# Performance work log

Measured on AMD Instinct MI355X. Metric: run time of the kernel, lower is better.

The kernel has to match this reference:

```python
import jax, jax.numpy as jnp
import numpy as np

HEADS = 8
DIM_HEAD = 64
SCALE = DIM_HEAD ** -0.5


def setup_inputs() -> dict:
    key = jax.random.key(0)
    ks = jax.random.split(key, 7)
    B, N, M, D, INNER = 2, 4096, 4096, 1024, HEADS * DIM_HEAD
    x = jax.random.normal(ks[0], (B, N, D), dtype=jnp.float32)
    context = jax.random.normal(ks[1], (B, M, D), dtype=jnp.float32)
    Wq = jax.random.normal(ks[2], (D, INNER), dtype=jnp.float32) * 0.02
    Wk = jax.random.normal(ks[3], (D, INNER), dtype=jnp.float32) * 0.02
    Wv = jax.random.normal(ks[4], (D, INNER), dtype=jnp.float32) * 0.02
    Wo = jax.random.normal(ks[5], (INNER, D), dtype=jnp.float32) * 0.02
    bo = jnp.zeros((D,), dtype=jnp.float32)
    return {"x": x, "context": context, "Wq": Wq, "Wk": Wk, "Wv": Wv, "Wo": Wo, "bo": bo}


def reference(x, context, Wq, Wk, Wv, Wo, bo):
    B, N, _ = x.shape
    M = context.shape[1]
    # projections (no bias, as in to_q/to_k/to_v)
    q = (x @ Wq).reshape(B, N, HEADS, DIM_HEAD)        # b n h d
    k = (context @ Wk).reshape(B, M, HEADS, DIM_HEAD)  # b m h d
    v = (context @ Wv).reshape(B, M, HEADS, DIM_HEAD)
    # scaled dot-product attention (the chunk loop in the original is math-equivalent)
    scores = jnp.einsum('bnhd,bmhd->bhnm', q, k) * SCALE
    attn = jax.nn.softmax(scores, axis=-1)
    out = jnp.einsum('bhnm,bmhd->bnhd', attn, v).reshape(B, N, HEADS * DIM_HEAD)
    # to_out: Linear with bias (dropout p=0.0 -> identity)
    return out @ Wo + bo
```

## Files before the change

kernel.cpp:

```cpp
#include <hip/hip_runtime.h>
#include <hip/hip_bf16.h>

typedef short bf16x8 __attribute__((ext_vector_type(8)));
typedef float f32x4 __attribute__((ext_vector_type(4)));
typedef float f32x16 __attribute__((ext_vector_type(16)));

#define MFMA16(a, b, c) __builtin_amdgcn_mfma_f32_16x16x32_bf16((a), (b), (c), 0, 0, 0)
#define MFMA32(a, b, c) __builtin_amdgcn_mfma_f32_32x32x16_bf16((a), (b), (c), 0, 0, 0)

#if __has_builtin(__builtin_amdgcn_exp2f)
#define EXP2(x) __builtin_amdgcn_exp2f(x)
#else
#define EXP2(x) __expf((x) * 0.6931471805599453f)
#endif

__device__ __forceinline__ ushort f2bf(float f) {
  union { float f; unsigned u; } x; x.f = f;
  unsigned u = x.u;
  return (ushort)((u + 0x7fffu + ((u >> 16) & 1u)) >> 16);
}

__device__ __forceinline__ unsigned cvtpk(float a, float b) {
  unsigned r;
  asm("v_cvt_pk_bf16_f32 %0, %1, %2" : "=v"(r) : "v"(a), "v"(b));
  return r;
}

__device__ __forceinline__ void plswap(unsigned& a, unsigned& b) {
  asm volatile("v_permlane32_swap_b32 %0, %1" : "+v"(a), "+v"(b));
}

__device__ __forceinline__ float bfbits2f(unsigned hw) {
  union { unsigned u; float f; } x; x.u = hw << 16; return x.f;
}

__device__ __forceinline__ void gl2lds16(const ushort* g, ushort* l) {
  typedef const __attribute__((address_space(1))) unsigned int* gp_t;
  typedef __attribute__((address_space(3))) unsigned int* lp_t;
  __builtin_amdgcn_global_load_lds((gp_t)(const void*)g, (lp_t)(void*)l, 16, 0, 0);
}

__global__ void transpose_all(const float* __restrict__ Wq, const float* __restrict__ Wk,
                              const float* __restrict__ Wv, const float* __restrict__ Wo,
                              ushort* __restrict__ Wqt, ushort* __restrict__ Wkt,
                              ushort* __restrict__ Wvt, ushort* __restrict__ Wot,
                              float qscale) {
  __shared__ float t[64][65];
  const int z = blockIdx.z;
  const float* src; ushort* dst; int R, C; float scale = 1.0f;
  if (z == 0)      { src = Wq; dst = Wqt; R = 1024; C = 512; scale = qscale; }
  else if (z == 1) { src = Wk; dst = Wkt; R = 1024; C = 512; }
  else if (z == 2) { src = Wv; dst = Wvt; R = 1024; C = 512; }
  else             { src = Wo; dst = Wot; R = 512;  C = 1024; }
  const int r0 = blockIdx.y * 64, c0 = blockIdx.x * 64;
  if (r0 >= R || c0 >= C) return;
  const int tid = threadIdx.x;
#pragma unroll
  for (int i = 0; i < 16; i++) {
    int idx = i * 256 + tid; int rr = idx >> 6, cc = idx & 63;
    t[rr][cc] = src[(size_t)(r0 + rr) * C + c0 + cc];
  }
  __syncthreads();
#pragma unroll
  for (int i = 0; i < 16; i++) {
    int idx = i * 256 + tid; int cc = idx >> 6, rr = idx & 63;
    dst[(size_t)(c0 + cc) * R + r0 + rr] = f2bf(t[rr][cc] * scale);
  }
}

template<int OUT, int AF32, int BF32>
__device__ __forceinline__ void gemm_core(ushort* lA, ushort* lB,
                                          const void* __restrict__ Av,
                                          const void* __restrict__ Bv,
                                          void* __restrict__ Cv,
                                          const float* __restrict__ bias,
                                          int N, int K, int row0, int col0) {
  const int tid = threadIdx.x;
  const int lane = tid & 63, wid = tid >> 6;
  const int lr = lane >> 3;
  const int cswz = ((lane & 7) ^ lr) << 3;
  const int clin = (lane & 7) << 3;
  const int wbyte = (clin * 2) ^ (lr << 4);
  const int wm = (wid >> 1) * 64, wn = (wid & 1) * 64;
  const int lo = lane & 15, hi = lane >> 4;

  const float* Af = (const float*)Av;
  const float* Bf = (const float*)Bv;

  float4 a0[4], a1[4], b0[4], b1[4];
  if (AF32) {
#pragma unroll
    for (int i = 0; i < 4; i++) {
      const float* p = Af + (size_t)(row0 + (i * 4 + wid) * 8 + lr) * K + clin;
      a0[i] = *(const float4*)p;
      a1[i] = *(const float4*)(p + 4);
    }
  }
  if (BF32) {
#pragma unroll
    for (int i = 0; i < 4; i++) {
      const float* p = Bf + (size_t)(col0 + (i * 4 + wid) * 8 + lr) * K + clin;
      b0[i] = *(const float4*)p;
      b1[i] = *(const float4*)(p + 4);
    }
  }

  f32x4 acc[4][4] = {};

  for (int k0 = 0; k0 < K; k0 += 64) {
    if (AF32) {
#pragma unroll
      for (int i = 0; i < 4; i++) {
        uint4 w;
        w.x = cvtpk(a0[i].x, a0[i].y);
        w.y = cvtpk(a0[i].z, a0[i].w);
        w.z = cvtpk(a1[i].x, a1[i].y);
        w.w = cvtpk(a1[i].z, a1[i].w);
        *(uint4*)((char*)lA + ((i * 4 + wid) * 8 + lr) * 128 + wbyte) = w;
      }
    } else {
      const ushort* A = (const ushort*)Av;
#pragma unroll
      for (int i = 0; i < 4; i++) {
        int g = i * 4 + wid;
        gl2lds16(A + (size_t)(row0 + g * 8 + lr) * K + k0 + cswz, &lA[g * 512]);
      }
    }
    if (BF32) {
#pragma unroll
      for (int i = 0; i < 4; i++) {
        uint4 w;
        w.x = cvtpk(b0[i].x, b0[i].y);
        w.y = cvtpk(b0[i].z, b0[i].w);
        w.z = cvtpk(b1[i].x, b1[i].y);
        w.w = cvtpk(b1[i].z, b1[i].w);
        *(uint4*)((char*)lB + ((i * 4 + wid) * 8 + lr) * 128 + wbyte) = w;
      }
    } else {
      const ushort* B = (const ushort*)Bv;
#pragma unroll
      for (int i = 0; i < 4; i++) {
        int g = i * 4 + wid;
        gl2lds16(B + (size_t)(col0 + g * 8 + lr) * K + k0 + cswz, &lB[g * 512]);
      }
    }
    __syncthreads();

    if (AF32 && k0 + 64 < K) {
#pragma unroll
      for (int i = 0; i < 4; i++) {
        const float* p = Af + (size_t)(row0 + (i * 4 + wid) * 8 + lr) * K + (k0 + 64) + clin;
        a0[i] = *(const float4*)p;
        a1[i] = *(const float4*)(p + 4);
      }
    }
    if (BF32 && k0 + 64 < K) {
#pragma unroll
      for (int i = 0; i < 4; i++) {
        const float* p = Bf + (size_t)(col0 + (i * 4 + wid) * 8 + lr) * K + (k0 + 64) + clin;
        b0[i] = *(const float4*)p;
        b1[i] = *(const float4*)(p + 4);
      }
    }

#pragma unroll
    for (int kk = 0; kk < 2; kk++) {
      bf16x8 af[4], bfr[4];
      const int kbyte = kk * 64 + hi * 16;
#pragma unroll
      for (int i = 0; i < 4; i++) {
        int r = wm + i * 16 + lo;
        af[i] = *(const bf16x8*)((const char*)lA + r * 128 + (kbyte ^ ((r & 7) << 4)));
        int c = wn + i * 16 + lo;
        bfr[i] = *(const bf16x8*)((const char*)lB + c * 128 + (kbyte ^ ((c & 7) << 4)));
      }
#pragma unroll
      for (int i = 0; i < 4; i++)
#pragma unroll
        for (int j = 0; j < 4; j++)
          acc[i][j] = MFMA16(bfr[j], af[i], acc[i][j]);
    }
    __syncthreads();
  }

#pragma unroll
  for (int i = 0; i < 4; i++)
#pragma unroll
    for (int j = 0; j < 4; j++) {
      const int row = row0 + wm + i * 16 + lo;
      const int col = col0 + wn + j * 16 + hi * 4;
      const f32x4 v = acc[i][j];
      if (OUT == 1) {
        const float4 bv = *(const float4*)(bias + col);
        float4 w;
        w.x = v[0] + bv.x; w.y = v[1] + bv.y; w.z = v[2] + bv.z; w.w = v[3] + bv.w;
        *(float4*)((float*)Cv + (size_t)row * N + col) = w;
      } else if (OUT == 0) {
        uint2 w; w.x = cvtpk(v[0], v[1]); w.y = cvtpk(v[2], v[3]);
        *(uint2*)((ushort*)Cv + (size_t)row * N + col) = w;
      } else {
        uint2 w; w.x = cvtpk(v[0], v[1]); w.y = cvtpk(v[2], v[3]);
        *(uint2*)((ushort*)Cv + ((size_t)(col >> 12) * 512 + row) * 4096 + (col & 4095)) = w;
      }
    }
}

__global__ __launch_bounds__(256, 3)
void proj_fused(const float* __restrict__ x, const float* __restrict__ ctx,
                const ushort* __restrict__ Wqt, const ushort* __restrict__ Wkt,
                const ushort* __restrict__ Wvt,
                ushort* __restrict__ Qb, ushort* __restrict__ Kb, ushort* __restrict__ Vtb) {
  __shared__ __align__(16) ushort lA[128 * 64];
  __shared__ __align__(16) ushort lB[128 * 64];
  const int bid = blockIdx.x;
  if (bid < 512) {
    const float* A    = bid < 256 ? x   : ctx;
    const ushort* Bt  = bid < 256 ? Wqt : Wkt;
    ushort* C         = bid < 256 ? Qb  : Kb;
    const int l = bid & 255;
    gemm_core<0, 1, 0>(lA, lB, A, Bt, C, nullptr, 512, 1024, (l & 63) * 128, (l >> 6) * 128);
  } else {
    const int l = bid - 512;
    gemm_core<2, 0, 1>(lA, lB, Wvt, ctx, Vtb, nullptr, 8192, 1024, (l & 3) * 128, (l >> 2) * 128);
  }
}

__global__ __launch_bounds__(256, 3)
void out_gemm(const ushort* __restrict__ Ob, const ushort* __restrict__ Wot,
              float* __restrict__ out, const float* __restrict__ bo) {
  __shared__ __align__(16) ushort lA[128 * 64];
  __shared__ __align__(16) ushort lB[128 * 64];
  gemm_core<1, 0, 0>(lA, lB, Ob, Wot, out, bo, 1024, 512, blockIdx.x * 128, blockIdx.y * 128);
}

__global__ __launch_bounds__(256, 4)
void attn_kernel(const ushort* __restrict__ Q, const ushort* __restrict__ Kp,
                 const ushort* __restrict__ Vt, unsigned* __restrict__ Opart,
                 float* __restrict__ Lpart) {
  __shared__ __align__(16) ushort kbuf[2][64 * 64];
  __shared__ __align__(16) ushort vbuf[2][64 * 64];

  const int tid = threadIdx.x;
  const int lane = tid & 63, wid = tid >> 6;
  const int bid = blockIdx.x;
  const int kvh = bid >> 9;
  const int b9 = bid & 511;
  const int bh = (b9 & 7) * 2 + (b9 >> 8);
  const int qblk = (b9 >> 3) & 31;
  const int b = bh >> 3, h = bh & 7;
  const int l31 = lane & 31, hi5 = lane >> 5;
  const int qrow = qblk * 128 + wid * 32 + l31;
  const size_t rowbase = (size_t)b * 4096;
  const int hoff = h * 64;
  const int kv0 = kvh * 1024;
  const int swzk = (l31 & 7) << 4;

  bf16x8 qf[4];
  {
    const ushort* qp = Q + (rowbase + qrow) * 512 + hoff + hi5 * 8;
    qf[0] = *(const bf16x8*)(qp);
    qf[1] = *(const bf16x8*)(qp + 16);
    qf[2] = *(const bf16x8*)(qp + 32);
    qf[3] = *(const bf16x8*)(qp + 48);
  }

  const int r0 = wid * 16 + (lane >> 3);
  const int r1 = r0 + 8;
  const int c00 = ((((lane & 7) * 16) ^ ((r0 & 7) << 4)) >> 1);
  const int c01 = ((((lane & 7) * 16) ^ ((r1 & 7) << 4)) >> 1);
  const ushort* kp0 = Kp + (rowbase + kv0 + r0) * 512 + hoff + c00;
  const ushort* kp1 = Kp + (rowbase + kv0 + r1) * 512 + hoff + c01;
  const ushort* vp0 = Vt + ((size_t)bh * 64 + r0) * 4096 + kv0 + c00;
  const ushort* vp1 = Vt + ((size_t)bh * 64 + r1) * 4096 + kv0 + c01;

  float l_run = 0.f;
  f32x16 o0 = {}, o1 = {};

  gl2lds16(kp0, &kbuf[0][wid * 1024]);
  gl2lds16(kp1, &kbuf[0][wid * 1024 + 512]);
  gl2lds16(vp0, &vbuf[0][wid * 1024]);
  gl2lds16(vp1, &vbuf[0][wid * 1024 + 512]);
  __syncthreads();

  for (int t = 0; t < 16; t++) {
    const int cur = t & 1;
    if (t < 15) {
      const size_t ko = (size_t)(t + 1) * (64 * 512);
      const int vo = (t + 1) * 64;
      gl2lds16(kp0 + ko, &kbuf[cur ^ 1][wid * 1024]);
      gl2lds16(kp1 + ko, &kbuf[cur ^ 1][wid * 1024 + 512]);
      gl2lds16(vp0 + vo, &vbuf[cur ^ 1][wid * 1024]);
      gl2lds16(vp1 + vo, &vbuf[cur ^ 1][wid * 1024 + 512]);
    }
    const char* kb = (const char*)kbuf[cur];
    const char* vb = (const char*)vbuf[cur];

    f32x16 s0 = {}, s1 = {};
    __builtin_amdgcn_s_setprio(1);
#pragma unroll
    for (int kt = 0; kt < 4; kt++) {
      bf16x8 kf = *(const bf16x8*)(kb + l31 * 128 + ((kt * 32 + hi5 * 16) ^ swzk));
      s0 = MFMA32(kf, qf[kt], s0);
    }
#pragma unroll
    for (int kt = 0; kt < 4; kt++) {
      bf16x8 kf = *(const bf16x8*)(kb + (32 + l31) * 128 + ((kt * 32 + hi5 * 16) ^ swzk));
      s1 = MFMA32(kf, qf[kt], s1);
    }
    __builtin_amdgcn_s_setprio(0);

#pragma unroll
    for (int i = 0; i < 16; i++) { s0[i] = EXP2(s0[i]); s1[i] = EXP2(s1[i]); }

    float sm[16];
#pragma unroll
    for (int i = 0; i < 8; i++) sm[i] = s0[2 * i] + s0[2 * i + 1];
#pragma unroll
    for (int i = 0; i < 8; i++) sm[8 + i] = s1[2 * i] + s1[2 * i + 1];
#pragma unroll
    for (int st = 8; st > 0; st >>= 1)
#pragma unroll
      for (int i = 0; i < st; i++) sm[i] = sm[2 * i] + sm[2 * i + 1];
    float rs = sm[0];
    rs += __shfl_xor(rs, 32);
    l_run += rs;

    unsigned p0[8], p1[8];
#pragma unroll
    for (int p = 0; p < 8; p++) {
      p0[p] = cvtpk(s0[2 * p], s0[2 * p + 1]);
      p1[p] = cvtpk(s1[2 * p], s1[2 * p + 1]);
    }
    plswap(p0[0], p0[2]); plswap(p0[1], p0[3]);
    plswap(p0[4], p0[6]); plswap(p0[5], p0[7]);
    plswap(p1[0], p1[2]); plswap(p1[1], p1[3]);
    plswap(p1[4], p1[6]); plswap(p1[5], p1[7]);

    union PF { unsigned u[4]; bf16x8 v; } pf[4];
    pf[0].u[0] = p0[0]; pf[0].u[1] = p0[1]; pf[0].u[2] = p0[2]; pf[0].u[3] = p0[3];
    pf[1].u[0] = p0[4]; pf[1].u[1] = p0[5]; pf[1].u[2] = p0[6]; pf[1].u[3] = p0[7];
    pf[2].u[0] = p1[0]; pf[2].u[1] = p1[1]; pf[2].u[2] = p1[2]; pf[2].u[3] = p1[3];
    pf[3].u[0] = p1[4]; pf[3].u[1] = p1[5]; pf[3].u[2] = p1[6]; pf[3].u[3] = p1[7];

    __builtin_amdgcn_s_setprio(1);
#pragma unroll
    for (int ks = 0; ks < 4; ks++) {
      bf16x8 v0 = *(const bf16x8*)(vb + l31 * 128 + ((ks * 32 + hi5 * 16) ^ swzk));
      bf16x8 v1 = *(const bf16x8*)(vb + (32 + l31) * 128 + ((ks * 32 + hi5 * 16) ^ swzk));
      o0 = MFMA32(v0, pf[ks].v, o0);
      o1 = MFMA32(v1, pf[ks].v, o1);
    }
    __builtin_amdgcn_s_setprio(0);

    __syncthreads();
  }

  const float inv = 1.0f / l_run;
  unsigned* op = Opart + ((size_t)kvh * 65536 + (size_t)bh * 4096 + qrow) * 32;
  {
    uint4 wa, wb;
    wa.x = cvtpk(o0[0] * inv, o0[1] * inv);
    wa.y = cvtpk(o0[2] * inv, o0[3] * inv);
    wa.z = cvtpk(o0[4] * inv, o0[5] * inv);
    wa.w = cvtpk(o0[6] * inv, o0[7] * inv);
    wb.x = cvtpk(o0[8] * inv, o0[9] * inv);
    wb.y = cvtpk(o0[10] * inv, o0[11] * inv);
    wb.z = cvtpk(o0[12] * inv, o0[13] * inv);
    wb.w = cvtpk(o0[14] * inv, o0[15] * inv);
    *(uint4*)(op + hi5 * 8) = wa;
    *(uint4*)(op + hi5 * 8 + 4) = wb;
    wa.x = cvtpk(o1[0] * inv, o1[1] * inv);
    wa.y = cvtpk(o1[2] * inv, o1[3] * inv);
    wa.z = cvtpk(o1[4] * inv, o1[5] * inv);
    wa.w = cvtpk(o1[6] * inv, o1[7] * inv);
    wb.x = cvtpk(o1[8] * inv, o1[9] * inv);
    wb.y = cvtpk(o1[10] * inv, o1[11] * inv);
    wb.z = cvtpk(o1[12] * inv, o1[13] * inv);
    wb.w = cvtpk(o1[14] * inv, o1[15] * inv);
    *(uint4*)(op + 16 + hi5 * 8) = wa;
    *(uint4*)(op + 16 + hi5 * 8 + 4) = wb;
  }
  if (hi5 == 0)
    Lpart[(size_t)kvh * 65536 + (size_t)bh * 4096 + qrow] = l_run;
}

__global__ __launch_bounds__(256)
void attn_merge(const unsigned* __restrict__ Opart, const float* __restrict__ Lpart,
                ushort* __restrict__ Ob) {
  const int idx = blockIdx.x * 256 + threadIdx.x;
  const int qg = idx >> 5, slot = idx & 31;
  float l0 = Lpart[qg];
  float l1 = Lpart[65536 + qg];
  float l2 = Lpart[2 * 65536 + qg];
  float l3 = Lpart[3 * 65536 + qg];
  const float inv = 1.0f / (l0 + l1 + l2 + l3);
  float ra = 0.f, rb = 0.f;
#pragma unroll
  for (int i = 0; i < 4; i++) {
    const float w = (i == 0 ? l0 : i == 1 ? l1 : i == 2 ? l2 : l3) * inv;
    const unsigned u = Opart[((size_t)i * 65536 + qg) * 32 + slot];
    ra += bfbits2f(u & 0xffffu) * w;
    rb += bfbits2f(u >> 16) * w;
  }
  const int dt = slot >> 4, s = slot & 15;
  const int h5 = s >> 3, p = s & 7;
  const int d0 = dt * 32 + 2 * (p & 1) + 8 * (p >> 1) + 4 * h5;
  const int bh = qg >> 12, qrow = qg & 4095;
  unsigned* dst = (unsigned*)(Ob + ((size_t)(bh >> 3) * 4096 + qrow) * 512 + (bh & 7) * 64 + d0);
  *dst = cvtpk(ra, rb);
}

extern "C" void kernel_launch(void* const* d_in, const int* in_sizes, int n_in,
                              void* d_out, int out_size, void* d_ws, size_t ws_size,
                              hipStream_t stream) {
  (void)in_sizes; (void)n_in; (void)out_size;
  const float* x   = (const float*)d_in[0];
  const float* ctx = (const float*)d_in[1];
  const float* Wq  = (const float*)d_in[2];
  const float* Wk  = (const float*)d_in[3];
  const float* Wv  = (const float*)d_in[4];
  const float* Wo  = (const float*)d_in[5];
  const float* bo  = (const float*)d_in[6];

  const float QSCALE = 0.125f * 1.4426950408889634f;
  const size_t MB = 1024 * 1024;
  if (ws_size < 72 * MB) return;
  char* ws = (char*)d_ws;
  ushort* Wqt = (ushort*)(ws + 0 * MB);
  ushort* Wkt = (ushort*)(ws + 1 * MB);
  ushort* Wvt = (ushort*)(ws + 2 * MB);
  ushort* Wot = (ushort*)(ws + 3 * MB);
  unsigned* Opart = (unsigned*)(ws + 4 * MB);
  float*    Lp    = (float*)(ws + 38 * MB);
  ushort* Qb   = (ushort*)(ws + 40 * MB);
  ushort* Kb   = (ushort*)(ws + 48 * MB);
  ushort* Vtb  = (ushort*)(ws + 56 * MB);
  ushort* Ob   = (ushort*)(ws + 64 * MB);

  transpose_all<<<dim3(16, 16, 4), dim3(256), 0, stream>>>(Wq, Wk, Wv, Wo,
                                                           Wqt, Wkt, Wvt, Wot, QSCALE);

  proj_fused<<<dim3(768), dim3(256), 0, stream>>>(x, ctx, Wqt, Wkt, Wvt, Qb, Kb, Vtb);

  attn_kernel<<<dim3(2048), dim3(256), 0, stream>>>(Qb, Kb, Vtb, Opart, Lp);
  attn_merge<<<dim3(8192), dim3(256), 0, stream>>>(Opart, Lp, Ob);

  out_gemm<<<dim3(64, 8), dim3(256), 0, stream>>>(Ob, Wot, (float*)d_out, bo);
}
```

Before: 157.4 us.

## Fuse split-KV attention merge into output projection GEMM A-tile load

Removes the separate attn_merge kernel and the bf16 Ob intermediate by having the output GEMM read the four partial attention outputs and their softmax denominators, combine them, and write the merged bf16 tile straight into shared memory. This saves a launch and the Ob write/read round trip. In exchange, each row block's merge is recomputed by all eight column blocks, multiplying partial-output reads. The A operand also becomes a synchronous scattered gather instead of an async copy.

```diff
diff --git a/kernel.cpp b/kernel.cpp
--- a/kernel.cpp
+++ b/kernel.cpp
@@ -226,11 +226,101 @@
 }
 
 __global__ __launch_bounds__(256, 3)
-void out_gemm(const ushort* __restrict__ Ob, const ushort* __restrict__ Wot,
-              float* __restrict__ out, const float* __restrict__ bo) {
+void out_gemm_fused(const unsigned* __restrict__ Opart, const float* __restrict__ Lpart,
+                    const ushort* __restrict__ Wot,
+                    float* __restrict__ out, const float* __restrict__ bo) {
   __shared__ __align__(16) ushort lA[128 * 64];
   __shared__ __align__(16) ushort lB[128 * 64];
-  gemm_core<1, 0, 0>(lA, lB, Ob, Wot, out, bo, 1024, 512, blockIdx.x * 128, blockIdx.y * 128);
+  const int tid = threadIdx.x;
+  const int lane = tid & 63, wid = tid >> 6;
+  const int lr = lane >> 3;
+  const int cswz = ((lane & 7) ^ lr) << 3;
+  const int clin = (lane & 7) << 3;
+  const int wbyte = (clin * 2) ^ (lr << 4);
+  const int wm = (wid >> 1) * 64, wn = (wid & 1) * 64;
+  const int lo = lane & 15, hi = lane >> 4;
+  const int row0 = blockIdx.x * 128, col0 = blockIdx.y * 128;
+  const int N = 1024, K = 512;
+  const int b = row0 >> 12;
+
+  int wj[4];
+#pragma unroll
+  for (int j = 0; j < 4; j++) {
+    const int d0 = clin + 2 * j;
+    const int dt = d0 >> 5, r5 = d0 & 31;
+    const int h5 = (r5 >> 2) & 1, rem = r5 - 4 * h5;
+    wj[j] = dt * 16 + h5 * 8 + ((rem >> 3) << 1) + ((rem >> 1) & 1);
+  }
+
+  f32x4 acc[4][4] = {};
+
+  for (int k0 = 0; k0 < K; k0 += 64) {
+    const int h = k0 >> 6;
+#pragma unroll
+    for (int i = 0; i < 4; i++) {
+      const int rr = (i * 4 + wid) * 8 + lr;
+      const size_t qg = (size_t)(((b * 8 + h) << 12) | ((row0 + rr) & 4095));
+      const float l0 = Lpart[qg];
+      const float l1 = Lpart[65536 + qg];
+      const float l2 = Lpart[2 * 65536 + qg];
+      const float l3 = Lpart[3 * 65536 + qg];
+      const float inv = 1.0f / (l0 + l1 + l2 + l3);
+      const float w0 = l0 * inv, w1 = l1 * inv, w2 = l2 * inv, w3 = l3 * inv;
+      const unsigned* base = Opart + qg * 32;
+      uint4 wv;
+      unsigned* pw = (unsigned*)&wv;
+#pragma unroll
+      for (int j = 0; j < 4; j++) {
+        const unsigned u0 = base[wj[j]];
+        const unsigned u1 = base[(size_t)1 * 65536 * 32 + wj[j]];
+        const unsigned u2 = base[(size_t)2 * 65536 * 32 + wj[j]];
+        const unsigned u3 = base[(size_t)3 * 65536 * 32 + wj[j]];
+        const float ra = bfbits2f(u0 & 0xffffu) * w0 + bfbits2f(u1 & 0xffffu) * w1
+                       + bfbits2f(u2 & 0xffffu) * w2 + bfbits2f(u3 & 0xffffu) * w3;
+        const float rb = bfbits2f(u0 >> 16) * w0 + bfbits2f(u1 >> 16) * w1
+                       + bfbits2f(u2 >> 16) * w2 + bfbits2f(u3 >> 16) * w3;
+        pw[j] = cvtpk(ra, rb);
+      }
+      *(uint4*)((char*)lA + rr * 128 + wbyte) = wv;
+    }
+#pragma unroll
+    for (int i = 0; i < 4; i++) {
+      int g = i * 4 + wid;
+      gl2lds16(Wot + (size_t)(col0 + g * 8 + lr) * K + k0 + cswz, &lB[g * 512]);
+    }
+    __syncthreads();
+#pragma unroll
+    for (int kk = 0; kk < 2; kk++) {
+      bf16x8 af[4], bfr[4];
+      const int kbyte = kk * 64 + hi * 16;
+#pragma unroll
+      for (int i = 0; i < 4; i++) {
+        int r = wm + i * 16 + lo;
+        af[i] = *(const bf16x8*)((const char*)lA + r * 128 + (kbyte ^ ((r & 7) << 4)));
+        int c = wn + i * 16 + lo;
+        bfr[i] = *(const bf16x8*)((const char*)lB + c * 128 + (kbyte ^ ((c & 7) << 4)));
+      }
+#pragma unroll
+      for (int i = 0; i < 4; i++)
+#pragma unroll
+        for (int j = 0; j < 4; j++)
+          acc[i][j] = MFMA16(bfr[j], af[i], acc[i][j]);
+    }
+    __syncthreads();
+  }
+
+#pragma unroll
+  for (int i = 0; i < 4; i++)
+#pragma unroll
+    for (int j = 0; j < 4; j++) {
+      const int row = row0 + wm + i * 16 + lo;
+      const int col = col0 + wn + j * 16 + hi * 4;
+      const f32x4 v = acc[i][j];
+      const float4 bv = *(const float4*)(bo + col);
+      float4 w;
+      w.x = v[0] + bv.x; w.y = v[1] + bv.y; w.z = v[2] + bv.z; w.w = v[3] + bv.w;
+      *(float4*)(out + (size_t)row * N + col) = w;
+    }
 }
 
 __global__ __launch_bounds__(256, 4)
@@ -384,32 +474,6 @@
     Lpart[(size_t)kvh * 65536 + (size_t)bh * 4096 + qrow] = l_run;
 }
 
-__global__ __launch_bounds__(256)
-void attn_merge(const unsigned* __restrict__ Opart, const float* __restrict__ Lpart,
-                ushort* __restrict__ Ob) {
-  const int idx = blockIdx.x * 256 + threadIdx.x;
-  const int qg = idx >> 5, slot = idx & 31;
-  float l0 = Lpart[qg];
-  float l1 = Lpart[65536 + qg];
-  float l2 = Lpart[2 * 65536 + qg];
-  float l3 = Lpart[3 * 65536 + qg];
-  const float inv = 1.0f / (l0 + l1 + l2 + l3);
-  float ra = 0.f, rb = 0.f;
-#pragma unroll
-  for (int i = 0; i < 4; i++) {
-    const float w = (i == 0 ? l0 : i == 1 ? l1 : i == 2 ? l2 : l3) * inv;
-    const unsigned u = Opart[((size_t)i * 65536 + qg) * 32 + slot];
-    ra += bfbits2f(u & 0xffffu) * w;
-    rb += bfbits2f(u >> 16) * w;
-  }
-  const int dt = slot >> 4, s = slot & 15;
-  const int h5 = s >> 3, p = s & 7;
-  const int d0 = dt * 32 + 2 * (p & 1) + 8 * (p >> 1) + 4 * h5;
-  const int bh = qg >> 12, qrow = qg & 4095;
-  unsigned* dst = (unsigned*)(Ob + ((size_t)(bh >> 3) * 4096 + qrow) * 512 + (bh & 7) * 64 + d0);
-  *dst = cvtpk(ra, rb);
-}
-
 extern "C" void kernel_launch(void* const* d_in, const int* in_sizes, int n_in,
                               void* d_out, int out_size, void* d_ws, size_t ws_size,
                               hipStream_t stream) {
@@ -435,7 +499,6 @@
   ushort* Qb   = (ushort*)(ws + 40 * MB);
   ushort* Kb   = (ushort*)(ws + 48 * MB);
   ushort* Vtb  = (ushort*)(ws + 56 * MB);
-  ushort* Ob   = (ushort*)(ws + 64 * MB);
 
   transpose_all<<<dim3(16, 16, 4), dim3(256), 0, stream>>>(Wq, Wk, Wv, Wo,
                                                            Wqt, Wkt, Wvt, Wot, QSCALE);
@@ -443,7 +506,6 @@
   proj_fused<<<dim3(768), dim3(256), 0, stream>>>(x, ctx, Wqt, Wkt, Wvt, Qb, Kb, Vtb);
 
   attn_kernel<<<dim3(2048), dim3(256), 0, stream>>>(Qb, Kb, Vtb, Opart, Lp);
-  attn_merge<<<dim3(8192), dim3(256), 0, stream>>>(Opart, Lp, Ob);
-
-  out_gemm<<<dim3(64, 8), dim3(256), 0, stream>>>(Ob, Wot, (float*)d_out, bo);
-}
+
+  out_gemm_fused<<<dim3(64, 8), dim3(256), 0, stream>>>(Opart, Lp, Wot, (float*)d_out, bo);
+}
```

Result: slower. 196.9 us (+25.1%).
